# Kernel tuning notes

Measured on AMD Instinct MI355X. Metric: run time of the kernel, lower is better.

## Reference

```python
import jax, jax.numpy as jnp
import numpy as np

EPS = 1e-6
NEG = 1e9

def _norm(x):
    # Normalizator math with alpha=1, gamma=0 (torch.std is unbiased -> ddof=1)
    m = jnp.mean(x, axis=-1, keepdims=True)
    s = jnp.std(x, axis=-1, ddof=1, keepdims=True)
    return (x - m) / (s + EPS)

def setup_inputs() -> dict:
    key = jax.random.key(0)
    ks = jax.random.split(key, 16)
    T, S, D, F, L = 4096, 4096, 512, 2048, 4
    sc = 1.0 / np.sqrt(D)
    scf = 1.0 / np.sqrt(F)
    return {
        "current_tgt_output": jax.random.normal(ks[0], (T, D), jnp.float32),
        "encoder_output": jax.random.normal(ks[1], (S, D), jnp.float32),
        "cross_mask": jax.random.randint(ks[2], (T, S), 0, 2).astype(jnp.float32),
        "Wq": jax.random.normal(ks[3], (L, D, D), jnp.float32) * sc,
        "Wk": jax.random.normal(ks[4], (L, D, D), jnp.float32) * sc,
        "Wv": jax.random.normal(ks[5], (L, D, D), jnp.float32) * sc,
        "Wo": jax.random.normal(ks[6], (L, D, D), jnp.float32) * sc,
        "Cq": jax.random.normal(ks[7], (L, D, D), jnp.float32) * sc,
        "Ck": jax.random.normal(ks[8], (L, D, D), jnp.float32) * sc,
        "Cv": jax.random.normal(ks[9], (L, D, D), jnp.float32) * sc,
        "Co": jax.random.normal(ks[10], (L, D, D), jnp.float32) * sc,
        "W1": jax.random.normal(ks[11], (L, D, F), jnp.float32) * sc,
        "W2": jax.random.normal(ks[12], (L, F, D), jnp.float32) * scf,
        "alpha": jnp.ones((1,), jnp.float32),
        "gamma": jnp.zeros((1,), jnp.float32),
        "input_ids": jax.random.randint(ks[13], (T,), 0, S),
        "training_step": T,
        "training_mode": 1,
    }

def reference(current_tgt_output, encoder_output, cross_mask, Wq, Wk, Wv, Wo,
              Cq, Ck, Cv, Co, W1, W2, alpha, gamma, input_ids,
              training_step, training_mode):
    T = training_step
    x = current_tgt_output[:T] if training_mode else current_tgt_output
    cm = cross_mask[:T]                                  # [T, S]
    # the python double-loop -> single vectorized gather: self_mask[i,k]=cross_mask[i, input_ids[k]]
    self_mask = cm[:, input_ids]                         # [T, T]
    sbias = (self_mask - 1.0) * NEG                      # additive mask bias
    cbias = (cm - 1.0) * NEG
    D = x.shape[-1]
    scale = 1.0 / jnp.sqrt(jnp.asarray(D, x.dtype))
    L = Wq.shape[0]
    for l in range(L):
        h = _norm(x)
        q, k, v = h @ Wq[l], h @ Wk[l], h @ Wv[l]
        a = jax.nn.softmax(q @ k.T * scale + sbias, axis=-1)
        x = x + (a @ v) @ Wo[l]
        h = _norm(x)
        q = h @ Cq[l]
        k, v = encoder_output @ Ck[l], encoder_output @ Cv[l]
        a = jax.nn.softmax(q @ k.T * scale + cbias, axis=-1)
        x = x + (a @ v) @ Co[l]
        h = _norm(x)
        x = x + jax.nn.relu(h @ W1[l]) @ W2[l]
    return alpha * _norm(x) + gamma
```

## Files before the change

kernel.cpp:

```cpp
#include <hip/hip_runtime.h>
#include <math.h>

typedef _Float16 half_t;
typedef unsigned int u32;
typedef unsigned short u16;
typedef float f32x4 __attribute__((ext_vector_type(4)));
typedef _Float16 f16x8 __attribute__((ext_vector_type(8)));
typedef _Float16 f16x4 __attribute__((ext_vector_type(4)));

#define T_DIM 4096
#define S_DIM 4096
#define D_DIM 512
#define F_DIM 2048
#define NLAYER 4
#define KVS ((size_t)4096 * 512)

__device__ __forceinline__ void gload16(const void* g, void* l) {
    __builtin_amdgcn_global_load_lds(
        (const __attribute__((address_space(1))) u32*)g,
        (__attribute__((address_space(3))) u32*)l, 16, 0, 0);
}

template<int N> __device__ __forceinline__ void wait_vm() {
    if constexpr (N == 0) asm volatile("s_waitcnt vmcnt(0)" ::: "memory");
    else if constexpr (N == 3) asm volatile("s_waitcnt vmcnt(3)" ::: "memory");
    else if constexpr (N == 4) asm volatile("s_waitcnt vmcnt(4)" ::: "memory");
    else if constexpr (N == 6) asm volatile("s_waitcnt vmcnt(6)" ::: "memory");
    else if constexpr (N == 8) asm volatile("s_waitcnt vmcnt(8)" ::: "memory");
}

template<int BN, int EPI>
__global__ __launch_bounds__(512)
void gemm_nt(const half_t* __restrict__ A, int lda,
             const half_t* __restrict__ B, int ldb,
             int N, int K, int gx,
             const float* __restrict__ Cin, float* __restrict__ Cout,
             half_t* __restrict__ D1, int ldd)
{
    constexpr int BM = 128, BK = 64;
    constexpr int NF = BN / 32;
    constexpr int LPT = 2 + BN / 64;
    constexpr int NSLOT = (BN == 64) ? 3 : 2;
    __shared__ half_t As[NSLOT][BM * BK];
    __shared__ half_t Bs[NSLOT][BN * BK];

    const int tid  = threadIdx.x;
    const int wave = tid >> 6;
    const int lane = tid & 63;

    const int nb  = gridDim.x;
    const int bid = blockIdx.x;
    const int nid = (bid & 7) * (nb >> 3) + (bid >> 3);
    const int bx  = nid % gx;
    const int by  = nid / gx;
    const int bm = by * BM, bn = bx * BN;

    const int wm = (wave >> 1) * 32;
    const int wn = (wave & 1) * (BN / 2);
    const int kq = lane >> 4;
    const int rr = lane & 15;
    const int scol = (((lane & 7) ^ (lane >> 3)) << 3);

    f32x4 acc[2][NF];
#pragma unroll
    for (int m = 0; m < 2; ++m)
#pragma unroll
        for (int n = 0; n < NF; ++n)
            acc[m][n] = f32x4{0.f, 0.f, 0.f, 0.f};

    auto stage = [&](int buf, int k0) {
#pragma unroll
        for (int c = 0; c < 2; ++c) {
            const int row = wave * 16 + c * 8 + (lane >> 3);
            gload16(A + (size_t)(bm + row) * lda + k0 + scol,
                    (char*)&As[buf][0] + (wave * 2 + c) * 1024 + lane * 16);
        }
        if constexpr (BN == 64) {
            const int row = wave * 8 + (lane >> 3);
            gload16(B + (size_t)(bn + row) * ldb + k0 + scol,
                    (char*)&Bs[buf][0] + wave * 1024 + lane * 16);
        } else {
#pragma unroll
            for (int c = 0; c < 2; ++c) {
                const int row = wave * 16 + c * 8 + (lane >> 3);
                gload16(B + (size_t)(bn + row) * ldb + k0 + scol,
                        (char*)&Bs[buf][0] + (wave * 2 + c) * 1024 + lane * 16);
            }
        }
    };

    const int nt = K / BK;
    stage(0, 0);
    if constexpr (NSLOT == 3) stage(1, BK);
    int cur = 0, pf = NSLOT - 1;
    for (int t = 0; t < nt; ++t) {
        if (t + 1 < nt) wait_vm<(NSLOT - 2) * LPT>(); else wait_vm<0>();
        __builtin_amdgcn_s_barrier();
        if (t + NSLOT - 1 < nt) stage(pf, (t + NSLOT - 1) * BK);
#pragma unroll
        for (int ks = 0; ks < 2; ++ks) {
            f16x8 af[2], bf[NF];
#pragma unroll
            for (int m = 0; m < 2; ++m) {
                const int r = wm + m * 16 + rr;
                af[m] = *(const f16x8*)&As[cur][r * BK + (((ks * 4 + kq) ^ (r & 7)) << 3)];
            }
#pragma unroll
            for (int n = 0; n < NF; ++n) {
                const int r = wn + n * 16 + rr;
                bf[n] = *(const f16x8*)&Bs[cur][r * BK + (((ks * 4 + kq) ^ (r & 7)) << 3)];
            }
#pragma unroll
            for (int m = 0; m < 2; ++m)
#pragma unroll
                for (int n = 0; n < NF; ++n)
                    acc[m][n] = __builtin_amdgcn_mfma_f32_16x16x32_f16(af[m], bf[n], acc[m][n], 0, 0, 0);
        }
        cur = (cur + 1 == NSLOT) ? 0 : cur + 1;
        pf  = (pf  + 1 == NSLOT) ? 0 : pf  + 1;
    }

    const int r0 = bm + wm + (lane >> 4) * 4;
#pragma unroll
    for (int m = 0; m < 2; ++m)
#pragma unroll
        for (int n = 0; n < NF; ++n) {
            const int c = bn + wn + n * 16 + rr;
            if (EPI == 1) {
#pragma unroll
                for (int i = 0; i < 4; ++i) {
                    const int r = r0 + m * 16 + i;
                    Cout[(size_t)r * N + c] = Cin[(size_t)r * N + c] + acc[m][n][i];
                }
            } else {
#pragma unroll
                for (int i = 0; i < 4; ++i)
                    D1[(size_t)(r0 + m * 16 + i) * ldd + c] = (half_t)acc[m][n][i];
            }
        }
}

template<int EPI, int SPLITK = 1, int P16 = 1>
__global__ __launch_bounds__(256)
void gemm97(const half_t* __restrict__ A, int lda,
            const half_t* __restrict__ B, int ldb,
            int K, int gx, half_t* __restrict__ D,
            float* __restrict__ Fout, int ldd,
            half_t* __restrict__ D2 = nullptr, half_t* __restrict__ D3 = nullptr)
{
    constexpr int BK = 32, NSLOT = 3, LPT = 4;
    __shared__ half_t As[NSLOT][128 * BK];
    __shared__ half_t Bs[NSLOT][128 * BK];

    const int tid  = threadIdx.x;
    const int wave = tid >> 6;
    const int lane = tid & 63;

    const int nb  = gridDim.x;
    const int bid = blockIdx.x;
    const int nid = (bid & 7) * (nb >> 3) + (bid >> 3);
    const int gy  = nb / (gx * SPLITK);
    const int bx  = nid % gx;
    const int tmp = nid / gx;
    const int by  = tmp % gy;
    const int kz  = tmp / gy;
    const int bm = by * 128, bn = bx * 128;

    const int Keff = K / SPLITK;
    A += (size_t)kz * Keff;
    B += (size_t)kz * Keff;

    const int wm = (wave >> 1) * 64;
    const int wn = (wave & 1) * 64;
    const int kq = lane >> 4;
    const int rr = lane & 15;
    const int srow = lane >> 2;
    const int scol = (((lane & 3) ^ ((lane >> 3) & 3)) << 3);
    const int kqa  = kq ^ ((rr >> 1) & 3);

    const half_t* Abase = A + (size_t)(bm + wave * 16 + srow) * lda + scol;
    const half_t* Bbase = B + (size_t)(bn + wave * 16 + srow) * ldb + scol;

    f32x4 acc[4][4];
#pragma unroll
    for (int m = 0; m < 4; ++m)
#pragma unroll
        for (int n = 0; n < 4; ++n)
            acc[m][n] = f32x4{0.f, 0.f, 0.f, 0.f};

    auto stage = [&](int buf, int k0) {
#pragma unroll
        for (int c = 0; c < 2; ++c)
            gload16(Abase + (size_t)c * 64 * lda + k0,
                    (char*)&As[buf][0] + c * 4096 + wave * 1024 + lane * 16);
#pragma unroll
        for (int c = 0; c < 2; ++c)
            gload16(Bbase + (size_t)c * 64 * ldb + k0,
                    (char*)&Bs[buf][0] + c * 4096 + wave * 1024 + lane * 16);
    };

    const int nt = Keff / BK;
    stage(0, 0);
    stage(1, BK);
    int cur = 0, pf = 2;
    for (int t = 0; t < nt; ++t) {
        if (t + 1 < nt) wait_vm<LPT>(); else wait_vm<0>();
        __builtin_amdgcn_s_barrier();
        if (t + 2 < nt) stage(pf, (t + 2) * BK);
        f16x8 af[4], bf[4];
#pragma unroll
        for (int m = 0; m < 4; ++m)
            af[m] = *(const f16x8*)&As[cur][(wm + m * 16 + rr) * BK + kqa * 8];
#pragma unroll
        for (int n = 0; n < 4; ++n)
            bf[n] = *(const f16x8*)&Bs[cur][(wn + n * 16 + rr) * BK + kqa * 8];
#pragma unroll
        for (int m = 0; m < 4; ++m)
#pragma unroll
            for (int n = 0; n < 4; ++n)
                acc[m][n] = __builtin_amdgcn_mfma_f32_16x16x32_f16(af[m], bf[n], acc[m][n], 0, 0, 0);
        cur = (cur == 2) ? 0 : cur + 1;
        pf  = (pf  == 2) ? 0 : pf + 1;
    }

    const int r0 = bm + wm + (lane >> 4) * 4;
    const int soff = kz * gx * 128;
#pragma unroll
    for (int m = 0; m < 4; ++m)
#pragma unroll
        for (int n = 0; n < 4; ++n) {
            const int c = bn + wn + n * 16 + rr;
            if constexpr (SPLITK > 1) {
#pragma unroll
                for (int i = 0; i < 4; ++i) {
                    const size_t r = r0 + m * 16 + i;
                    if constexpr (P16) D[r * ldd + soff + c] = (half_t)acc[m][n][i];
                    else               Fout[r * ldd + soff + c] = acc[m][n][i];
                }
            } else if (EPI == 5) {
                if (bn < 512) {
#pragma unroll
                    for (int i = 0; i < 4; ++i)
                        D[(size_t)(r0 + m * 16 + i) * 512 + c] = (half_t)acc[m][n][i];
                } else if (bn < 1024) {
#pragma unroll
                    for (int i = 0; i < 4; ++i)
                        D2[(size_t)(r0 + m * 16 + i) * 512 + (c - 512)] = (half_t)acc[m][n][i];
                } else {
                    f16x4 hv;
#pragma unroll
                    for (int i = 0; i < 4; ++i) hv[i] = (half_t)acc[m][n][i];
                    *(f16x4*)&D3[(size_t)(c - 1024) * ldd + r0 + m * 16] = hv;
                }
            } else if (EPI == 7) {
                const int l = c >> 10;
                const int sub = c & 1023;
                if (sub < 512) {
#pragma unroll
                    for (int i = 0; i < 4; ++i)
                        D2[l * KVS + (size_t)(r0 + m * 16 + i) * 512 + sub] = (half_t)acc[m][n][i];
                } else {
                    f16x4 hv;
#pragma unroll
                    for (int i = 0; i < 4; ++i) hv[i] = (half_t)acc[m][n][i];
                    *(f16x4*)&D3[l * KVS + (size_t)(sub - 512) * ldd + r0 + m * 16] = hv;
                }
            } else {
#pragma unroll
                for (int i = 0; i < 4; ++i) {
                    float v = acc[m][n][i];
                    if (EPI == 4) v = fmaxf(v, 0.f);
                    D[(size_t)(r0 + m * 16 + i) * ldd + c] = (half_t)v;
                }
            }
        }
}

__global__ __launch_bounds__(256)
void reduce_p16(const half_t* __restrict__ P, half_t* __restrict__ ao)
{
    const size_t q = ((size_t)blockIdx.x * 256 + threadIdx.x) * 8;
    const size_t r = q >> 9;
    const int d = (int)(q & 511);
    const half_t* row = P + r * 2048 + d;
    float s[8] = {0.f};
#pragma unroll
    for (int j = 0; j < 4; ++j) {
        f16x8 v = *(const f16x8*)(row + j * 512);
#pragma unroll
        for (int e = 0; e < 8; ++e) s[e] += (float)v[e];
    }
    f16x8 o;
#pragma unroll
    for (int e = 0; e < 8; ++e) o[e] = (half_t)s[e];
    *(f16x8*)&ao[q] = o;
}

template<int FINAL>
__global__ __launch_bounds__(256)
void norm_red(const float* __restrict__ xin, const float* __restrict__ P,
              float* __restrict__ xbuf, half_t* __restrict__ hh,
              float* __restrict__ outF, const float* __restrict__ alphaP,
              const float* __restrict__ gammaP)
{
    const int row  = blockIdx.x * 4 + (threadIdx.x >> 6);
    const int lane = threadIdx.x & 63;
    const int d0 = lane * 8;
    const float* xr = xin + (size_t)row * D_DIM + d0;
    float v[8];
    {
        float4 a = *(const float4*)xr;
        float4 b = *(const float4*)(xr + 4);
        v[0]=a.x; v[1]=a.y; v[2]=a.z; v[3]=a.w; v[4]=b.x; v[5]=b.y; v[6]=b.z; v[7]=b.w;
    }
    const float* pr = P + (size_t)row * 2048 + d0;
#pragma unroll
    for (int j = 0; j < 4; ++j) {
        float4 a = *(const float4*)(pr + j * 512);
        float4 b = *(const float4*)(pr + j * 512 + 4);
        v[0]+=a.x; v[1]+=a.y; v[2]+=a.z; v[3]+=a.w; v[4]+=b.x; v[5]+=b.y; v[6]+=b.z; v[7]+=b.w;
    }
    if (!FINAL) {
        float* xo = xbuf + (size_t)row * D_DIM + d0;
        *(float4*)xo       = float4{v[0], v[1], v[2], v[3]};
        *(float4*)(xo + 4) = float4{v[4], v[5], v[6], v[7]};
    }
    float s = 0.f;
#pragma unroll
    for (int j = 0; j < 8; ++j) s += v[j];
#pragma unroll
    for (int off = 32; off; off >>= 1) s += __shfl_xor(s, off);
    const float mean = s * (1.f / 512.f);
    float ss = 0.f;
#pragma unroll
    for (int j = 0; j < 8; ++j) { float d = v[j] - mean; ss += d * d; }
#pragma unroll
    for (int off = 32; off; off >>= 1) ss += __shfl_xor(ss, off);
    const float inv = 1.f / (sqrtf(ss * (1.f / 511.f)) + 1e-6f);
    if (FINAL) {
        const float alp = alphaP[0], gam = gammaP[0];
        float o[8];
#pragma unroll
        for (int j = 0; j < 8; ++j) o[j] = alp * ((v[j] - mean) * inv) + gam;
        float* op = outF + (size_t)row * D_DIM + d0;
        *(float4*)op       = float4{o[0], o[1], o[2], o[3]};
        *(float4*)(op + 4) = float4{o[4], o[5], o[6], o[7]};
    } else {
        f16x8 hv;
#pragma unroll
        for (int j = 0; j < 8; ++j) hv[j] = (half_t)((v[j] - mean) * inv);
        *(f16x8*)&hh[(size_t)row * D_DIM + d0] = hv;
    }
}

template<int FINAL>
__global__ __launch_bounds__(256)
void norm_rows(const float* __restrict__ x, half_t* __restrict__ hh,
               float* __restrict__ outF, const float* __restrict__ alphaP,
               const float* __restrict__ gammaP)
{
    const int row  = blockIdx.x * 4 + (threadIdx.x >> 6);
    const int lane = threadIdx.x & 63;
    const float* xr = x + (size_t)row * D_DIM + lane * 8;
    float4 a = *(const float4*)xr;
    float4 b = *(const float4*)(xr + 4);
    float v[8] = {a.x, a.y, a.z, a.w, b.x, b.y, b.z, b.w};
    float s = 0.f;
#pragma unroll
    for (int j = 0; j < 8; ++j) s += v[j];
#pragma unroll
    for (int off = 32; off; off >>= 1) s += __shfl_xor(s, off);
    const float mean = s * (1.f / 512.f);
    float ss = 0.f;
#pragma unroll
    for (int j = 0; j < 8; ++j) { float d = v[j] - mean; ss += d * d; }
#pragma unroll
    for (int off = 32; off; off >>= 1) ss += __shfl_xor(ss, off);
    const float inv = 1.f / (sqrtf(ss * (1.f / 511.f)) + 1e-6f);
    if (FINAL) {
        const float alp = alphaP[0], gam = gammaP[0];
        float o[8];
#pragma unroll
        for (int j = 0; j < 8; ++j) o[j] = alp * ((v[j] - mean) * inv) + gam;
        float* op = outF + (size_t)row * D_DIM + lane * 8;
        *(float4*)op       = float4{o[0], o[1], o[2], o[3]};
        *(float4*)(op + 4) = float4{o[4], o[5], o[6], o[7]};
    } else {
        f16x8 hv;
#pragma unroll
        for (int j = 0; j < 8; ++j) hv[j] = (half_t)((v[j] - mean) * inv);
        *(f16x8*)&hh[(size_t)row * D_DIM + lane * 8] = hv;
    }
}

__global__ __launch_bounds__(256)
void cast_f16(const float* __restrict__ in, half_t* __restrict__ out)
{
    size_t i = ((size_t)blockIdx.x * 256 + threadIdx.x) * 8;
    float4 a = *(const float4*)&in[i];
    float4 b = *(const float4*)&in[i + 4];
    float v[8] = {a.x, a.y, a.z, a.w, b.x, b.y, b.z, b.w};
    f16x8 o;
#pragma unroll
    for (int j = 0; j < 8; ++j) o[j] = (half_t)v[j];
    *(f16x8*)&out[i] = o;
}

__global__ __launch_bounds__(256)
void transpose_cast8(const float* __restrict__ i0, const float* __restrict__ i1,
                     const float* __restrict__ i2, const float* __restrict__ i3,
                     const float* __restrict__ i4, const float* __restrict__ i5,
                     const float* __restrict__ i6, const float* __restrict__ i7,
                     half_t* __restrict__ o0, half_t* __restrict__ o1,
                     half_t* __restrict__ o2, half_t* __restrict__ o3,
                     half_t* __restrict__ o4, half_t* __restrict__ o5,
                     half_t* __restrict__ o6, half_t* __restrict__ o7,
                     float qscale)
{
    const int SQ = 512 * 512, QKVZ = 1536 * 512, KVZ = 1024 * 512;
    const int z = blockIdx.z, t = z >> 2, l = z & 3;
    const float* in; half_t* out; float sc = 1.f; int outZ;
    switch (t) {
        case 0: in = i0; out = o0; sc = qscale; outZ = QKVZ; break;
        case 1: in = i1; out = o1; outZ = QKVZ; break;
        case 2: in = i2; out = o2; outZ = QKVZ; break;
        case 3: in = i3; out = o3; outZ = SQ; break;
        case 4: in = i4; out = o4; sc = qscale; outZ = SQ; break;
        case 5: in = i5; out = o5; outZ = KVZ; break;
        case 6: in = i6; out = o6; outZ = KVZ; break;
        default: in = i7; out = o7; outZ = SQ; break;
    }
    in  += (size_t)l * SQ;
    out += (size_t)l * outZ;
    __shared__ float tile[32][33];
    const int tx = threadIdx.x & 31, ty = threadIdx.x >> 5;
    const int r0 = blockIdx.y * 32, c0 = blockIdx.x * 32;
#pragma unroll
    for (int i = 0; i < 4; ++i)
        tile[ty + i * 8][tx] = in[(size_t)(r0 + ty + i * 8) * 512 + c0 + tx];
    __syncthreads();
#pragma unroll
    for (int i = 0; i < 4; ++i)
        out[(size_t)(c0 + ty + i * 8) * 512 + r0 + tx] = (half_t)(tile[tx][ty + i * 8] * sc);
}

__global__ __launch_bounds__(256)
void transpose_cast(const float* __restrict__ in, half_t* __restrict__ out,
                    int R, int C, float scale, int inZ, int outZ)
{
    in  += (size_t)blockIdx.z * inZ;
    out += (size_t)blockIdx.z * outZ;
    __shared__ float tile[32][33];
    const int tx = threadIdx.x & 31, ty = threadIdx.x >> 5;
    const int r0 = blockIdx.y * 32, c0 = blockIdx.x * 32;
#pragma unroll
    for (int i = 0; i < 4; ++i)
        tile[ty + i * 8][tx] = in[(size_t)(r0 + ty + i * 8) * C + c0 + tx];
    __syncthreads();
#pragma unroll
    for (int i = 0; i < 4; ++i)
        out[(size_t)(c0 + ty + i * 8) * R + r0 + tx] = (half_t)(tile[tx][ty + i * 8] * scale);
}

__global__ __launch_bounds__(256)
void pack_masks(const float* __restrict__ cm, const int* __restrict__ ids,
                u32* __restrict__ crossb, u32* __restrict__ selfb)
{
    const int t = blockIdx.x;
    const float* row = cm + (size_t)t * S_DIM;
    __shared__ u32 cb[S_DIM / 32];
    __shared__ u16 sh16[256];
    const int tid = threadIdx.x;
    u32 bits = 0;
#pragma unroll
    for (int q = 0; q < 4; ++q) {
        float4 v = *(const float4*)&row[tid * 16 + q * 4];
        bits |= (v.x > 0.5f ? 1u : 0u) << (q * 4 + 0);
        bits |= (v.y > 0.5f ? 1u : 0u) << (q * 4 + 1);
        bits |= (v.z > 0.5f ? 1u : 0u) << (q * 4 + 2);
        bits |= (v.w > 0.5f ? 1u : 0u) << (q * 4 + 3);
    }
    ((u16*)cb)[tid] = (u16)bits;
    __syncthreads();
    u32 sb = 0;
#pragma unroll
    for (int q = 0; q < 4; ++q) {
        int4 id4 = *(const int4*)&ids[tid * 16 + q * 4];
        sb |= ((cb[id4.x >> 5] >> (id4.x & 31)) & 1u) << (q * 4 + 0);
        sb |= ((cb[id4.y >> 5] >> (id4.y & 31)) & 1u) << (q * 4 + 1);
        sb |= ((cb[id4.z >> 5] >> (id4.z & 31)) & 1u) << (q * 4 + 2);
        sb |= ((cb[id4.w >> 5] >> (id4.w & 31)) & 1u) << (q * 4 + 3);
    }
    sh16[tid] = (u16)sb;
    __syncthreads();
    if (tid < 128) {
        crossb[(size_t)t * 128 + tid] = cb[tid];
        selfb[(size_t)t * 128 + tid]  = (u32)sh16[2 * tid] | ((u32)sh16[2 * tid + 1] << 16);
    }
}

__global__ __launch_bounds__(256)
void softmax_rows16(half_t* __restrict__ logits, const u32* __restrict__ bits)
{
    const int t = blockIdx.x;
    half_t* row = logits + (size_t)t * S_DIM;
    const u32* bw = bits + (size_t)t * (S_DIM / 32);
    __shared__ float red[8];
    const int tid = threadIdx.x, wave = tid >> 6, lane = tid & 63;
    const int s0 = tid * 16;
    f16x8 h0 = *(const f16x8*)&row[s0];
    f16x8 h1 = *(const f16x8*)&row[s0 + 8];
    const u32 w = bw[tid >> 1] >> ((tid & 1) * 16);
    float z[16];
    float lmax = -3.0e38f;
#pragma unroll
    for (int q = 0; q < 16; ++q) {
        const float v = (float)((q < 8) ? h0[q & 7] : h1[q & 7]);
        z[q] = v + (((w >> q) & 1u) ? 0.f : -1e9f);
        lmax = fmaxf(lmax, z[q]);
    }
#pragma unroll
    for (int off = 32; off; off >>= 1) lmax = fmaxf(lmax, __shfl_xor(lmax, off));
    if (lane == 0) red[wave] = lmax;
    __syncthreads();
    const float mx = fmaxf(fmaxf(red[0], red[1]), fmaxf(red[2], red[3]));
    float lsum = 0.f;
#pragma unroll
    for (int q = 0; q < 16; ++q) { z[q] = __expf(z[q] - mx); lsum += z[q]; }
#pragma unroll
    for (int off = 32; off; off >>= 1) lsum += __shfl_xor(lsum, off);
    if (lane == 0) red[4 + wave] = lsum;
    __syncthreads();
    const float inv = 1.f / (red[4] + red[5] + red[6] + red[7]);
    f16x8 o0, o1;
#pragma unroll
    for (int q = 0; q < 8; ++q) {
        o0[q] = (half_t)(z[q] * inv);
        o1[q] = (half_t)(z[q + 8] * inv);
    }
    *(f16x8*)&row[s0] = o0;
    *(f16x8*)&row[s0 + 8] = o1;
}

extern "C" void kernel_launch(void* const* d_in, const int* in_sizes, int n_in,
                              void* d_out, int out_size, void* d_ws, size_t ws_size,
                              hipStream_t stream)
{
    (void)in_sizes; (void)n_in; (void)out_size; (void)ws_size;

    const float* x0p  = (const float*)d_in[0];
    const float* encp = (const float*)d_in[1];
    const float* cmp  = (const float*)d_in[2];
    const float* Wq = (const float*)d_in[3], *Wk = (const float*)d_in[4];
    const float* Wv = (const float*)d_in[5], *Wo = (const float*)d_in[6];
    const float* Cq = (const float*)d_in[7], *Ck = (const float*)d_in[8];
    const float* Cv = (const float*)d_in[9], *Co = (const float*)d_in[10];
    const float* W1p = (const float*)d_in[11];
    const float* W2p = (const float*)d_in[12];
    const float* alphap = (const float*)d_in[13];
    const float* gammap = (const float*)d_in[14];
    const int*   idsp   = (const int*)d_in[15];
    float* outp = (float*)d_out;

    char* wp = (char*)d_ws;
    auto take = [&](size_t nelem, int esz) -> void* {
        void* p = (void*)wp;
        wp += (nelem * (size_t)esz + 255) & ~(size_t)255;
        return p;
    };
    half_t* wqkvT = (half_t*)take((size_t)NLAYER * 1536 * 512, 2);
    half_t* ckvT  = (half_t*)take((size_t)NLAYER * 1024 * 512, 2);
    half_t* cqT   = (half_t*)take((size_t)NLAYER * 512 * 512, 2);
    half_t* woT   = (half_t*)take((size_t)NLAYER * 512 * 512, 2);
    half_t* coT   = (half_t*)take((size_t)NLAYER * 512 * 512, 2);
    half_t* w1T   = (half_t*)take((size_t)NLAYER * D_DIM * F_DIM, 2);
    half_t* w2T   = (half_t*)take((size_t)NLAYER * D_DIM * F_DIM, 2);
    half_t* hh    = (half_t*)take((size_t)T_DIM * D_DIM, 2);
    half_t* qb    = (half_t*)take((size_t)T_DIM * D_DIM, 2);
    half_t* kb    = (half_t*)take((size_t)S_DIM * D_DIM, 2);
    half_t* vT    = (half_t*)take((size_t)S_DIM * D_DIM, 2);
    half_t* ao    = (half_t*)take((size_t)T_DIM * D_DIM, 2);
    half_t* mid   = (half_t*)take((size_t)T_DIM * F_DIM, 2);
    half_t* enc16 = (half_t*)take((size_t)S_DIM * D_DIM, 2);
    half_t* kbC   = (half_t*)take((size_t)NLAYER * S_DIM * D_DIM, 2);
    half_t* vTC   = (half_t*)take((size_t)NLAYER * S_DIM * D_DIM, 2);
    float* xbuf   = (float*)take((size_t)T_DIM * D_DIM, 4);
    half_t* logit16 = (half_t*)take((size_t)T_DIM * S_DIM, 2);
    half_t* p16   = (half_t*)take((size_t)T_DIM * 2048, 2);
    float* pbuf   = (float*)take((size_t)T_DIM * 2048, 4);
    u32* crossb = (u32*)take((size_t)T_DIM * (S_DIM / 32), 4);
    u32* selfb  = (u32*)take((size_t)T_DIM * (S_DIM / 32), 4);

    const dim3 B(256), B512(512);
    const float qscale = 0.04419417382415922f;

    const int SQ = 512 * 512, QKVZ = 1536 * 512, FZ = 512 * 2048;
    transpose_cast8<<<dim3(16, 16, 32), B, 0, stream>>>(
        Wq, Wk, Wv, Wo, Cq, Ck, Cv, Co,
        wqkvT, wqkvT + SQ, wqkvT + 2 * SQ, woT, cqT, ckvT, ckvT + SQ, coT, qscale);
    transpose_cast<<<dim3(64,16,4), B, 0, stream>>>(W1p, w1T, 512, 2048, 1.f, FZ, FZ);
    transpose_cast<<<dim3(16,64,4), B, 0, stream>>>(W2p, w2T, 2048, 512, 1.f, FZ, FZ);
    cast_f16<<<dim3((S_DIM * D_DIM / 8) / 256), B, 0, stream>>>(encp, enc16);
    pack_masks<<<dim3(T_DIM), B, 0, stream>>>(cmp, idsp, crossb, selfb);
    gemm97<7><<<dim3(1024), B, 0, stream>>>(enc16, 512, ckvT, 512,
        512, 32, nullptr, nullptr, 4096, kbC, vTC);

    for (int l = 0; l < NLAYER; ++l) {
        const float* xin = (l == 0) ? x0p : xbuf;

        if (l == 0)
            norm_rows<0><<<T_DIM / 4, B, 0, stream>>>(x0p, hh, nullptr, nullptr, nullptr);
        else
            norm_red<0><<<T_DIM / 4, B, 0, stream>>>(xbuf, pbuf, xbuf, hh, nullptr, nullptr, nullptr);

        gemm97<5><<<dim3(384), B, 0, stream>>>(hh, 512, wqkvT + (size_t)l * QKVZ, 512,
            512, 12, qb, nullptr, 4096, kb, vT);
        gemm97<2><<<dim3(1024), B, 0, stream>>>(qb, 512, kb, 512, 512, 32, logit16, nullptr, 4096);
        softmax_rows16<<<dim3(T_DIM), B, 0, stream>>>(logit16, selfb);
        gemm97<0, 4, 1><<<dim3(512), B, 0, stream>>>(logit16, 4096, vT, 4096,
            4096, 4, p16, nullptr, 2048);
        reduce_p16<<<dim3(1024), B, 0, stream>>>(p16, ao);
        gemm_nt<64, 1><<<dim3(256), B512, 0, stream>>>(ao, 512, woT + (size_t)l * SQ, 512,
            512, 512, 8, xin, xbuf, nullptr, 0);

        norm_rows<0><<<T_DIM / 4, B, 0, stream>>>(xbuf, hh, nullptr, nullptr, nullptr);
        gemm_nt<64, 2><<<dim3(256), B512, 0, stream>>>(hh, 512, cqT + (size_t)l * SQ, 512,
            512, 512, 8, nullptr, nullptr, qb, 512);
        gemm97<2><<<dim3(1024), B, 0, stream>>>(qb, 512, kbC + (size_t)l * KVS, 512,
            512, 32, logit16, nullptr, 4096);
        softmax_rows16<<<dim3(T_DIM), B, 0, stream>>>(logit16, crossb);
        gemm97<0, 4, 1><<<dim3(512), B, 0, stream>>>(logit16, 4096, vTC + (size_t)l * KVS, 4096,
            4096, 4, p16, nullptr, 2048);
        reduce_p16<<<dim3(1024), B, 0, stream>>>(p16, ao);
        gemm_nt<64, 1><<<dim3(256), B512, 0, stream>>>(ao, 512, coT + (size_t)l * SQ, 512,
            512, 512, 8, xbuf, xbuf, nullptr, 0);

        norm_rows<0><<<T_DIM / 4, B, 0, stream>>>(xbuf, hh, nullptr, nullptr, nullptr);
        gemm97<4><<<dim3(512), B, 0, stream>>>(hh, 512, w1T + (size_t)l * FZ, 512,
            512, 16, mid, nullptr, 2048);
        gemm97<0, 4, 0><<<dim3(512), B, 0, stream>>>(mid, 2048, w2T + (size_t)l * FZ, 2048,
            2048, 4, nullptr, pbuf, 2048);
    }

    norm_red<1><<<T_DIM / 4, B, 0, stream>>>(xbuf, pbuf, xbuf, nullptr, outp, alphap, gammap);
}
```

Measured before the change: 1.070 ms.

## Split-K attention PV and output projections, fuse residual add into norm

Raises split-K of the attention P@V GEMMs from 4 to 8, doubling the grid and partial buffer, with the reduction kernel now templated on the split count. The Wo/Co projections also become split-K by 2 and write fp32 partials instead of adding the residual in the epilogue. A new norm_red2 kernel then sums the residual and both partials and normalizes in one pass, replacing the separate norm_rows launch. The aim is more parallelism on these small-grid GEMMs, at the cost of extra partial-buffer memory traffic.

```diff
diff --git a/kernel.cpp b/kernel.cpp
--- a/kernel.cpp
+++ b/kernel.cpp
@@ -29,12 +29,12 @@
     else if constexpr (N == 8) asm volatile("s_waitcnt vmcnt(8)" ::: "memory");
 }
 
-template<int BN, int EPI>
+template<int BN, int EPI, int SPLITK = 1>
 __global__ __launch_bounds__(512)
 void gemm_nt(const half_t* __restrict__ A, int lda,
              const half_t* __restrict__ B, int ldb,
              int N, int K, int gx,
-             const float* __restrict__ Cin, float* __restrict__ Cout,
+             float* __restrict__ Cout,
              half_t* __restrict__ D1, int ldd)
 {
     constexpr int BM = 128, BK = 64;
@@ -51,9 +51,16 @@
     const int nb  = gridDim.x;
     const int bid = blockIdx.x;
     const int nid = (bid & 7) * (nb >> 3) + (bid >> 3);
+    const int gy  = nb / (gx * SPLITK);
     const int bx  = nid % gx;
-    const int by  = nid / gx;
+    const int tmp = nid / gx;
+    const int by  = tmp % gy;
+    const int kz  = tmp / gy;
     const int bm = by * BM, bn = bx * BN;
+
+    const int Keff = K / SPLITK;
+    A += (size_t)kz * Keff;
+    B += (size_t)kz * Keff;
 
     const int wm = (wave >> 1) * 32;
     const int wn = (wave & 1) * (BN / 2);
@@ -89,7 +96,7 @@
         }
     };
 
-    const int nt = K / BK;
+    const int nt = Keff / BK;
     stage(0, 0);
     if constexpr (NSLOT == 3) stage(1, BK);
     int cur = 0, pf = NSLOT - 1;
@@ -126,12 +133,10 @@
 #pragma unroll
         for (int n = 0; n < NF; ++n) {
             const int c = bn + wn + n * 16 + rr;
-            if (EPI == 1) {
-#pragma unroll
-                for (int i = 0; i < 4; ++i) {
-                    const int r = r0 + m * 16 + i;
-                    Cout[(size_t)r * N + c] = Cin[(size_t)r * N + c] + acc[m][n][i];
-                }
+            if (EPI == 0) {
+#pragma unroll
+                for (int i = 0; i < 4; ++i)
+                    Cout[(size_t)(r0 + m * 16 + i) * (SPLITK * 512) + kz * 512 + c] = acc[m][n][i];
             } else {
 #pragma unroll
                 for (int i = 0; i < 4; ++i)
@@ -276,16 +281,17 @@
         }
 }
 
+template<int NS>
 __global__ __launch_bounds__(256)
 void reduce_p16(const half_t* __restrict__ P, half_t* __restrict__ ao)
 {
     const size_t q = ((size_t)blockIdx.x * 256 + threadIdx.x) * 8;
     const size_t r = q >> 9;
     const int d = (int)(q & 511);
-    const half_t* row = P + r * 2048 + d;
+    const half_t* row = P + r * (NS * 512) + d;
     float s[8] = {0.f};
 #pragma unroll
-    for (int j = 0; j < 4; ++j) {
+    for (int j = 0; j < NS; ++j) {
         f16x8 v = *(const f16x8*)(row + j * 512);
 #pragma unroll
         for (int e = 0; e < 8; ++e) s[e] += (float)v[e];
@@ -351,6 +357,49 @@
         for (int j = 0; j < 8; ++j) hv[j] = (half_t)((v[j] - mean) * inv);
         *(f16x8*)&hh[(size_t)row * D_DIM + d0] = hv;
     }
+}
+
+__global__ __launch_bounds__(256)
+void norm_red2(const float* __restrict__ xin, const float* __restrict__ P,
+               float* __restrict__ xbuf, half_t* __restrict__ hh)
+{
+    const int row  = blockIdx.x * 4 + (threadIdx.x >> 6);
+    const int lane = threadIdx.x & 63;
+    const int d0 = lane * 8;
+    const float* xr = xin + (size_t)row * D_DIM + d0;
+    float v[8];
+    {
+        float4 a = *(const float4*)xr;
+        float4 b = *(const float4*)(xr + 4);
+        v[0]=a.x; v[1]=a.y; v[2]=a.z; v[3]=a.w; v[4]=b.x; v[5]=b.y; v[6]=b.z; v[7]=b.w;
+    }
+    const float* pr = P + (size_t)row * 1024 + d0;
+#pragma unroll
+    for (int j = 0; j < 2; ++j) {
+        float4 a = *(const float4*)(pr + j * 512);
+        float4 b = *(const float4*)(pr + j * 512 + 4);
+        v[0]+=a.x; v[1]+=a.y; v[2]+=a.z; v[3]+=a.w; v[4]+=b.x; v[5]+=b.y; v[6]+=b.z; v[7]+=b.w;
+    }
+    float* xo = xbuf + (size_t)row * D_DIM + d0;
+    *(float4*)xo       = float4{v[0], v[1], v[2], v[3]};
+    *(float4*)(xo + 4) = float4{v[4], v[5], v[6], v[7]};
+
+    float s = 0.f;
+#pragma unroll
+    for (int j = 0; j < 8; ++j) s += v[j];
+#pragma unroll
+    for (int off = 32; off; off >>= 1) s += __shfl_xor(s, off);
+    const float mean = s * (1.f / 512.f);
+    float ss = 0.f;
+#pragma unroll
+    for (int j = 0; j < 8; ++j) { float d = v[j] - mean; ss += d * d; }
+#pragma unroll
+    for (int off = 32; off; off >>= 1) ss += __shfl_xor(ss, off);
+    const float inv = 1.f / (sqrtf(ss * (1.f / 511.f)) + 1e-6f);
+    f16x8 hv;
+#pragma unroll
+    for (int j = 0; j < 8; ++j) hv[j] = (half_t)((v[j] - mean) * inv);
+    *(f16x8*)&hh[(size_t)row * D_DIM + d0] = hv;
 }
 
 template<int FINAL>
@@ -586,7 +635,8 @@
     half_t* vTC   = (half_t*)take((size_t)NLAYER * S_DIM * D_DIM, 2);
     float* xbuf   = (float*)take((size_t)T_DIM * D_DIM, 4);
     half_t* logit16 = (half_t*)take((size_t)T_DIM * S_DIM, 2);
-    half_t* p16   = (half_t*)take((size_t)T_DIM * 2048, 2);
+    half_t* p16   = (half_t*)take((size_t)T_DIM * 4096, 2);
+    float* pbufA  = (float*)take((size_t)T_DIM * 1024, 4);
     float* pbuf   = (float*)take((size_t)T_DIM * 2048, 4);
     u32* crossb = (u32*)take((size_t)T_DIM * (S_DIM / 32), 4);
     u32* selfb  = (u32*)take((size_t)T_DIM * (S_DIM / 32), 4);
@@ -617,25 +667,25 @@
             512, 12, qb, nullptr, 4096, kb, vT);
         gemm97<2><<<dim3(1024), B, 0, stream>>>(qb, 512, kb, 512, 512, 32, logit16, nullptr, 4096);
         softmax_rows16<<<dim3(T_DIM), B, 0, stream>>>(logit16, selfb);
-        gemm97<0, 4, 1><<<dim3(512), B, 0, stream>>>(logit16, 4096, vT, 4096,
-            4096, 4, p16, nullptr, 2048);
-        reduce_p16<<<dim3(1024), B, 0, stream>>>(p16, ao);
-        gemm_nt<64, 1><<<dim3(256), B512, 0, stream>>>(ao, 512, woT + (size_t)l * SQ, 512,
-            512, 512, 8, xin, xbuf, nullptr, 0);
-
-        norm_rows<0><<<T_DIM / 4, B, 0, stream>>>(xbuf, hh, nullptr, nullptr, nullptr);
+        gemm97<0, 8, 1><<<dim3(1024), B, 0, stream>>>(logit16, 4096, vT, 4096,
+            4096, 4, p16, nullptr, 4096);
+        reduce_p16<8><<<dim3(1024), B, 0, stream>>>(p16, ao);
+        gemm_nt<64, 0, 2><<<dim3(512), B512, 0, stream>>>(ao, 512, woT + (size_t)l * SQ, 512,
+            512, 512, 8, pbufA, nullptr, 0);
+
+        norm_red2<<<T_DIM / 4, B, 0, stream>>>(xin, pbufA, xbuf, hh);
         gemm_nt<64, 2><<<dim3(256), B512, 0, stream>>>(hh, 512, cqT + (size_t)l * SQ, 512,
-            512, 512, 8, nullptr, nullptr, qb, 512);
+            512, 512, 8, nullptr, qb, 512);
         gemm97<2><<<dim3(1024), B, 0, stream>>>(qb, 512, kbC + (size_t)l * KVS, 512,
             512, 32, logit16, nullptr, 4096);
         softmax_rows16<<<dim3(T_DIM), B, 0, stream>>>(logit16, crossb);
-        gemm97<0, 4, 1><<<dim3(512), B, 0, stream>>>(logit16, 4096, vTC + (size_t)l * KVS, 4096,
-            4096, 4, p16, nullptr, 2048);
-        reduce_p16<<<dim3(1024), B, 0, stream>>>(p16, ao);
-        gemm_nt<64, 1><<<dim3(256), B512, 0, stream>>>(ao, 512, coT + (size_t)l * SQ, 512,
-            512, 512, 8, xbuf, xbuf, nullptr, 0);
-
-        norm_rows<0><<<T_DIM / 4, B, 0, stream>>>(xbuf, hh, nullptr, nullptr, nullptr);
+        gemm97<0, 8, 1><<<dim3(1024), B, 0, stream>>>(logit16, 4096, vTC + (size_t)l * KVS, 4096,
+            4096, 4, p16, nullptr, 4096);
+        reduce_p16<8><<<dim3(1024), B, 0, stream>>>(p16, ao);
+        gemm_nt<64, 0, 2><<<dim3(512), B512, 0, stream>>>(ao, 512, coT + (size_t)l * SQ, 512,
+            512, 512, 8, pbufA, nullptr, 0);
+
+        norm_red2<<<T_DIM / 4, B, 0, stream>>>(xbuf, pbufA, xbuf, hh);
         gemm97<4><<<dim3(512), B, 0, stream>>>(hh, 512, w1T + (size_t)l * FZ, 512,
             512, 16, mid, nullptr, 2048);
         gemm97<0, 4, 0><<<dim3(512), B, 0, stream>>>(mid, 2048, w2T + (size_t)l * FZ, 2048,
```

New measurement: 1.124 ms. 5.0% more time.
